# Optimization experiments

Hardware: AMD Instinct MI355X
Metric: run time of the kernel (lower is better)

The kernel has to match this reference:

```python
import jax, jax.numpy as jnp
import numpy as np

NUM_HEADS = 12


def setup_inputs() -> dict:
    key = jax.random.key(0)
    k0, k1, k2 = jax.random.split(key, 3)
    B, S, D = 2, 2048, 1536
    scale = 1.0 / np.sqrt(D)
    return {
        "hidden_states": jax.random.normal(k0, (B, S, D), dtype=jnp.float32),
        "W_fc": jax.random.normal(k1, (D, D), dtype=jnp.float32) * scale,
        "b_fc": jnp.zeros((D,), dtype=jnp.float32),
        "W_proj": jax.random.normal(k2, (D, D), dtype=jnp.float32) * scale,
        "b_proj": jnp.zeros((D,), dtype=jnp.float32),
    }


def reference(hidden_states, W_fc, b_fc, W_proj, b_proj):
    B, S, D = hidden_states.shape
    H = NUM_HEADS
    hd = D // H
    # value_states: [B, H, S, hd] (key_states == value_states in the original)
    v = (hidden_states @ W_fc.T + b_fc).reshape(B, S, H, hd).transpose(0, 2, 1, 3)
    # Uniform-weight causal sliding-window attention, window_h = 2^(h+1)-1.
    i = jnp.arange(S)[:, None]          # query pos
    j = jnp.arange(S)[None, :]          # key pos
    w = (2 ** jnp.arange(1, H + 1, dtype=jnp.int32) - 1)[:, None, None]  # [H,1,1]
    mask = (j <= i) & (j >= i - w + 1)                                    # [H,S,S]
    valid_len = jnp.minimum(i + 1, w).astype(v.dtype)                     # [H,S,1]
    attn = jnp.where(mask, 1.0 / valid_len, 0.0)                          # [H,S,S]
    # [H,S,S] x [B,H,S,hd] -> [B,S,H,hd] -> [B,S,D]
    out = jnp.einsum("hqk,bhkd->bqhd", attn, v).reshape(B, S, D)
    attn_weights = jnp.broadcast_to(attn[None], (B, H, S, S))
    return out @ W_proj.T + b_proj, attn_weights
```

## Files before the change

kernel.cpp:

```cpp
#include <hip/hip_runtime.h>
#include <hip/hip_bf16.h>

#define S_LEN   2048
#define DMODEL  1536
#define NBATCH  2
#define NHEADS  12
#define MROWS   (NBATCH * S_LEN)
#define NCHUNK  64
#define CHUNK   32

#define NGEMM_BLK  384
#define AW_BLK     3072
#define AW_TOTAL4  25165824u

#define AW_G1   10223616u
#define AW_PF    1572864u
#define AW_WA    3932160u
#define AW_G2    9437184u

#define PF_BLK   768
#define PF_AWBLK 1536
#define WA_BLK   3072
#define WA_AWBLK 1536

typedef unsigned short u16;
typedef __attribute__((ext_vector_type(8))) short bf16x8;
typedef __attribute__((ext_vector_type(4))) float f32x4;

__device__ __forceinline__ u16 f2bf(float x) {
  unsigned u = __float_as_uint(x);
  u += 0x7fffu + ((u >> 16) & 1u);
  return (u16)(u >> 16);
}
__device__ __forceinline__ float bf2f(u16 x) {
  return __uint_as_float(((unsigned)x) << 16);
}

__device__ __forceinline__ void aw_stream(f32x4* __restrict__ aw, unsigned aw0,
                                          unsigned awcnt, unsigned blk, unsigned nblk) {
  const unsigned stride = nblk * 256u;
  const unsigned end = aw0 + awcnt;
  unsigned t = aw0 + blk * 256u + threadIdx.x;
  for (; t < end; t += stride) {
    int j0 = (int)(t & 511u) << 2;
    int i  = (int)(t >> 9) & (S_LEN - 1);
    int bh = (int)(t >> 20);
    int h  = bh >= NHEADS ? bh - NHEADS : bh;
    int w  = (2 << h) - 1;
    int len = min(i + 1, w);
    float inv = 1.0f / (float)len;
    int lo = i - w + 1;
    f32x4 r;
    r.x = (j0     <= i && j0     >= lo) ? inv : 0.f;
    r.y = (j0 + 1 <= i && j0 + 1 >= lo) ? inv : 0.f;
    r.z = (j0 + 2 <= i && j0 + 2 >= lo) ? inv : 0.f;
    r.w = (j0 + 3 <= i && j0 + 3 >= lo) ? inv : 0.f;
    __builtin_nontemporal_store(r, &aw[t]);
  }
}

#define N4_HID  1572864
#define N4_W    589824
__global__ void cvt_all(const float4* __restrict__ h, const float4* __restrict__ wf,
                        const float4* __restrict__ wp, ushort4* __restrict__ ho,
                        ushort4* __restrict__ wfo, ushort4* __restrict__ wpo) {
  int t = blockIdx.x * blockDim.x + threadIdx.x;
  const float4* src;
  ushort4* dst;
  int idx;
  if (t < N4_HID)            { src = h;  dst = ho;  idx = t; }
  else if (t < N4_HID + N4_W){ src = wf; dst = wfo; idx = t - N4_HID; }
  else                       { src = wp; dst = wpo; idx = t - N4_HID - N4_W; }
  float4 f = src[idx];
  ushort4 o;
  o.x = f2bf(f.x); o.y = f2bf(f.y); o.z = f2bf(f.z); o.w = f2bf(f.w);
  dst[idx] = o;
}

__device__ __forceinline__ void gld_lds16(u16* lds, const u16* g) {
  __builtin_amdgcn_global_load_lds(
      (const __attribute__((address_space(1))) unsigned int*)g,
      (__attribute__((address_space(3))) unsigned int*)lds, 16, 0, 0);
}

template <bool WITH_CSUM, typename CT>
__global__ __launch_bounds__(256)
void gemm_aw(const u16* __restrict__ A, const u16* __restrict__ B,
             const float* __restrict__ bias, CT* __restrict__ C,
             float* __restrict__ cs, f32x4* __restrict__ aw,
             unsigned aw0, unsigned awcnt, int Ndim, int Kdim) {
  if ((int)blockIdx.x >= NGEMM_BLK) {
    aw_stream(aw, aw0, awcnt, blockIdx.x - NGEMM_BLK, gridDim.x - NGEMM_BLK);
    return;
  }

  __shared__ __align__(16) u16 As[2][128 * 32];
  __shared__ __align__(16) u16 Bs[2][128 * 32];
  __shared__ float colpart[4][128];

  const int tid  = threadIdx.x;
  const int wave = tid >> 6;
  const int lane = tid & 63;
  const int l15  = lane & 15;
  const int quad = lane >> 4;
  const int bm = (blockIdx.x / (DMODEL / 128)) * 128;
  const int bn = (blockIdx.x % (DMODEL / 128)) * 128;
  const int wm = (wave >> 1) * 64;
  const int wn = (wave & 1) * 64;

  f32x4 acc[4][4] = {};

  const int srow = wave * 32 + (lane >> 2);
  const int skk  = (lane & 3) * 8;
  const u16* gA = A + (size_t)(bm + srow) * Kdim + skk;
  const u16* gB = B + (size_t)(bn + srow) * Kdim + skk;
  const int lofs = (wave * 32) * 32;
  const size_t rstep16 = (size_t)16 * Kdim;

  gld_lds16(&As[0][lofs],           gA);
  gld_lds16(&As[0][lofs + 16 * 32], gA + rstep16);
  gld_lds16(&Bs[0][lofs],           gB);
  gld_lds16(&Bs[0][lofs + 16 * 32], gB + rstep16);

  int cur = 0;
  for (int k0 = 0; k0 < Kdim; k0 += 32) {
    __syncthreads();
    if (k0 + 32 < Kdim) {
      const int nxt = cur ^ 1;
      gld_lds16(&As[nxt][lofs],           gA + k0 + 32);
      gld_lds16(&As[nxt][lofs + 16 * 32], gA + k0 + 32 + rstep16);
      gld_lds16(&Bs[nxt][lofs],           gB + k0 + 32);
      gld_lds16(&Bs[nxt][lofs + 16 * 32], gB + k0 + 32 + rstep16);
    }

    bf16x8 af[4], bfr[4];
#pragma unroll
    for (int i = 0; i < 4; ++i)
      af[i] = *(const bf16x8*)&As[cur][(wm + i * 16 + l15) * 32 + quad * 8];
#pragma unroll
    for (int j = 0; j < 4; ++j)
      bfr[j] = *(const bf16x8*)&Bs[cur][(wn + j * 16 + l15) * 32 + quad * 8];
#pragma unroll
    for (int i = 0; i < 4; ++i)
#pragma unroll
      for (int j = 0; j < 4; ++j)
        acc[i][j] = __builtin_amdgcn_mfma_f32_16x16x32_bf16(af[i], bfr[j], acc[i][j], 0, 0, 0);
    cur ^= 1;
  }

  const int r0 = quad * 4;
#pragma unroll
  for (int j = 0; j < 4; ++j) {
    const int col = bn + wn + j * 16 + l15;
    const float bj = bias[col];
    float sA = 0.f, sB = 0.f;
#pragma unroll
    for (int i = 0; i < 4; ++i) {
      const int row = bm + wm + i * 16 + r0;
#pragma unroll
      for (int r = 0; r < 4; ++r) {
        float cv = acc[i][j][r] + bj;
        if constexpr (sizeof(CT) == 2) {
          C[(size_t)(row + r) * Ndim + col] = (CT)f2bf(cv);
        } else {
          __builtin_nontemporal_store((CT)cv, &C[(size_t)(row + r) * Ndim + col]);
        }
        if (WITH_CSUM) { if (i < 2) sA += cv; else sB += cv; }
      }
    }
    if (WITH_CSUM) {
      sA += __shfl_xor(sA, 16); sA += __shfl_xor(sA, 32);
      sB += __shfl_xor(sB, 16); sB += __shfl_xor(sB, 32);
      if (quad == 0) {
        colpart[(wm >> 5) | 0][wn + j * 16 + l15] = sA;
        colpart[(wm >> 5) | 1][wn + j * 16 + l15] = sB;
      }
    }
  }
  if (WITH_CSUM) {
    __syncthreads();
    if (tid < 128) {
      const int b  = bm >> 11;
      const int c0 = (bm & 2047) >> 5;
#pragma unroll
      for (int g = 0; g < 4; ++g)
        cs[((size_t)b * NCHUNK + c0 + g) * DMODEL + bn + tid] = colpart[g][tid];
    }
  }
}

__global__ void chunk_prefix_aw(const float* __restrict__ cs, float* __restrict__ E,
                                f32x4* __restrict__ aw, unsigned aw0, unsigned awcnt) {
  if ((int)blockIdx.x >= PF_BLK) {
    aw_stream(aw, aw0, awcnt, blockIdx.x - PF_BLK, PF_AWBLK);
    return;
  }
  int t = blockIdx.x * blockDim.x + threadIdx.x;
  int d = t % DMODEL;
  int c = (t / DMODEL) % NCHUNK;
  int b = t / (DMODEL * NCHUNK);
  const float* p = cs + (size_t)b * NCHUNK * DMODEL + d;
  float s = 0.f;
  for (int cc = 0; cc < c; ++cc) s += p[(size_t)cc * DMODEL];
  E[t] = s;
}

__global__ void winavg_aw(const u16* __restrict__ v, const float* __restrict__ E,
                          u16* __restrict__ A2,
                          f32x4* __restrict__ aw, unsigned aw0, unsigned awcnt) {
  if ((int)blockIdx.x >= WA_BLK) {
    aw_stream(aw, aw0, awcnt, blockIdx.x - WA_BLK, WA_AWBLK);
    return;
  }
  int t = blockIdx.x * blockDim.x + threadIdx.x;
  int d = t % DMODEL;
  int s = (t / DMODEL) & 255;
  int b = t / (DMODEL * 256);
  const int h = d >> 7;
  const int w = (2 << h) - 1;
  const u16* vb  = v + (size_t)b * S_LEN * DMODEL + d;
  const float* Eb = E + (size_t)b * NCHUNK * DMODEL + d;

  const int i0 = s * 8;
  float lead = Eb[(size_t)(i0 >> 5) * DMODEL];
  for (int r = i0 & ~31; r < i0; ++r)
    lead += bf2f(vb[(size_t)r * DMODEL]);

  float trail = 0.f;
  if (i0 + 7 >= w) {
    const int jf = max(i0, w) - w;
    if (jf > 0) {
      const int ct = (jf - 1) >> 5;
      trail = Eb[(size_t)ct * DMODEL];
      for (int r = ct * 32; r < jf; ++r)
        trail += bf2f(vb[(size_t)r * DMODEL]);
    }
  }

  u16* out = A2 + ((size_t)(b * S_LEN + i0)) * DMODEL + d;
#pragma unroll
  for (int rr = 0; rr < 8; ++rr) {
    const int i = i0 + rr;
    lead += bf2f(vb[(size_t)i * DMODEL]);
    float o;
    if (i < w) {
      o = lead / (float)(i + 1);
    } else {
      trail += bf2f(vb[(size_t)(i - w) * DMODEL]);
      o = (lead - trail) / (float)w;
    }
    out[(size_t)rr * DMODEL] = f2bf(o);
  }
}

extern "C" void kernel_launch(void* const* d_in, const int* in_sizes, int n_in,
                              void* d_out, int out_size, void* d_ws, size_t ws_size,
                              hipStream_t stream) {
  const float* hidden = (const float*)d_in[0];
  const float* W_fc   = (const float*)d_in[1];
  const float* b_fc   = (const float*)d_in[2];
  const float* W_proj = (const float*)d_in[3];
  const float* b_proj = (const float*)d_in[4];
  float* outp = (float*)d_out;
  f32x4* aw = (f32x4*)(outp + (size_t)MROWS * DMODEL);

  char* ws = (char*)d_ws;
  u16*   A16   = (u16*)(ws);
  u16*   Wfc16 = (u16*)(ws + 12582912);
  u16*   Wpj16 = (u16*)(ws + 17301504);
  u16*   v16   = (u16*)(ws + 22020096);
  float* csums = (float*)(ws + 34603008);
  float* Epre  = (float*)(ws + 35389440);

  cvt_all<<<10752, 256, 0, stream>>>((const float4*)hidden, (const float4*)W_fc,
                                     (const float4*)W_proj, (ushort4*)A16,
                                     (ushort4*)Wfc16, (ushort4*)Wpj16);

  gemm_aw<true, u16><<<NGEMM_BLK + AW_BLK, 256, 0, stream>>>(
      A16, Wfc16, b_fc, v16, csums, aw, 0u, AW_G1, DMODEL, DMODEL);

  chunk_prefix_aw<<<PF_BLK + PF_AWBLK, 256, 0, stream>>>(
      csums, Epre, aw, AW_G1, AW_PF);

  winavg_aw<<<WA_BLK + WA_AWBLK, 256, 0, stream>>>(
      v16, Epre, A16, aw, AW_G1 + AW_PF, AW_WA);

  gemm_aw<false, float><<<NGEMM_BLK + AW_BLK, 256, 0, stream>>>(
      A16, Wpj16, b_proj, outp, nullptr, aw, AW_G1 + AW_PF + AW_WA, AW_G2, DMODEL, DMODEL);
}
```

Baseline: 532.8 us.

## Drop chunk-prefix kernel, fold prefix sums into winavg, rebalance attn-weight streaming

Removes the separate chunk_prefix kernel: winavg now sums the per-chunk column sums directly, computing both the lead and trail prefixes in one pass. Attention-weight writing is widened to 8 floats per thread, and part of it moves into the conversion kernel, with the split across the four remaining launches re-tuned. This saves one launch and the round trip through the E buffer, and spreads the large output write over more of the timeline. In exchange each winavg thread makes up to 64 strided column-sum reads instead of one, which is redundant work.

```diff
diff --git a/kernel.cpp b/kernel.cpp
--- a/kernel.cpp
+++ b/kernel.cpp
@@ -7,21 +7,20 @@
 #define NHEADS  12
 #define MROWS   (NBATCH * S_LEN)
 #define NCHUNK  64
-#define CHUNK   32
 
 #define NGEMM_BLK  384
+
+#define AW_TOT8   12582912u
+#define AW_CVT8    1048576u
+#define AW_G1_8    4718592u
+#define AW_WA8     2359296u
+#define AW_G2_8    4456448u
+
+#define CVT_BLK    10752
+#define CVT_AWBLK  1024
 #define AW_BLK     3072
-#define AW_TOTAL4  25165824u
-
-#define AW_G1   10223616u
-#define AW_PF    1572864u
-#define AW_WA    3932160u
-#define AW_G2    9437184u
-
-#define PF_BLK   768
-#define PF_AWBLK 1536
-#define WA_BLK   3072
-#define WA_AWBLK 1536
+#define WA_BLK     3072
+#define WA_AWBLK   2048
 
 typedef unsigned short u16;
 typedef __attribute__((ext_vector_type(8))) short bf16x8;
@@ -36,26 +35,29 @@
   return __uint_as_float(((unsigned)x) << 16);
 }
 
-__device__ __forceinline__ void aw_stream(f32x4* __restrict__ aw, unsigned aw0,
-                                          unsigned awcnt, unsigned blk, unsigned nblk) {
+__device__ __forceinline__ void aw_stream8(f32x4* __restrict__ aw, unsigned aw0,
+                                           unsigned awcnt, unsigned blk, unsigned nblk) {
   const unsigned stride = nblk * 256u;
   const unsigned end = aw0 + awcnt;
-  unsigned t = aw0 + blk * 256u + threadIdx.x;
-  for (; t < end; t += stride) {
-    int j0 = (int)(t & 511u) << 2;
-    int i  = (int)(t >> 9) & (S_LEN - 1);
-    int bh = (int)(t >> 20);
+  for (unsigned t = aw0 + blk * 256u + threadIdx.x; t < end; t += stride) {
+    int j0 = (int)(t & 255u) << 3;
+    int i  = (int)(t >> 8) & (S_LEN - 1);
+    int bh = (int)(t >> 19);
     int h  = bh >= NHEADS ? bh - NHEADS : bh;
     int w  = (2 << h) - 1;
-    int len = min(i + 1, w);
-    float inv = 1.0f / (float)len;
+    float inv = 1.0f / (float)min(i + 1, w);
     int lo = i - w + 1;
-    f32x4 r;
-    r.x = (j0     <= i && j0     >= lo) ? inv : 0.f;
-    r.y = (j0 + 1 <= i && j0 + 1 >= lo) ? inv : 0.f;
-    r.z = (j0 + 2 <= i && j0 + 2 >= lo) ? inv : 0.f;
-    r.w = (j0 + 3 <= i && j0 + 3 >= lo) ? inv : 0.f;
-    __builtin_nontemporal_store(r, &aw[t]);
+    f32x4 r0, r1;
+    r0.x = (j0     <= i && j0     >= lo) ? inv : 0.f;
+    r0.y = (j0 + 1 <= i && j0 + 1 >= lo) ? inv : 0.f;
+    r0.z = (j0 + 2 <= i && j0 + 2 >= lo) ? inv : 0.f;
+    r0.w = (j0 + 3 <= i && j0 + 3 >= lo) ? inv : 0.f;
+    r1.x = (j0 + 4 <= i && j0 + 4 >= lo) ? inv : 0.f;
+    r1.y = (j0 + 5 <= i && j0 + 5 >= lo) ? inv : 0.f;
+    r1.z = (j0 + 6 <= i && j0 + 6 >= lo) ? inv : 0.f;
+    r1.w = (j0 + 7 <= i && j0 + 7 >= lo) ? inv : 0.f;
+    __builtin_nontemporal_store(r0, &aw[2u * t]);
+    __builtin_nontemporal_store(r1, &aw[2u * t + 1u]);
   }
 }
 
@@ -63,7 +65,12 @@
 #define N4_W    589824
 __global__ void cvt_all(const float4* __restrict__ h, const float4* __restrict__ wf,
                         const float4* __restrict__ wp, ushort4* __restrict__ ho,
-                        ushort4* __restrict__ wfo, ushort4* __restrict__ wpo) {
+                        ushort4* __restrict__ wfo, ushort4* __restrict__ wpo,
+                        f32x4* __restrict__ aw, unsigned aw0, unsigned awcnt) {
+  if ((int)blockIdx.x >= CVT_BLK) {
+    aw_stream8(aw, aw0, awcnt, blockIdx.x - CVT_BLK, CVT_AWBLK);
+    return;
+  }
   int t = blockIdx.x * blockDim.x + threadIdx.x;
   const float4* src;
   ushort4* dst;
@@ -90,7 +97,7 @@
              float* __restrict__ cs, f32x4* __restrict__ aw,
              unsigned aw0, unsigned awcnt, int Ndim, int Kdim) {
   if ((int)blockIdx.x >= NGEMM_BLK) {
-    aw_stream(aw, aw0, awcnt, blockIdx.x - NGEMM_BLK, gridDim.x - NGEMM_BLK);
+    aw_stream8(aw, aw0, awcnt, blockIdx.x - NGEMM_BLK, gridDim.x - NGEMM_BLK);
     return;
   }
 
@@ -189,27 +196,11 @@
   }
 }
 
-__global__ void chunk_prefix_aw(const float* __restrict__ cs, float* __restrict__ E,
-                                f32x4* __restrict__ aw, unsigned aw0, unsigned awcnt) {
-  if ((int)blockIdx.x >= PF_BLK) {
-    aw_stream(aw, aw0, awcnt, blockIdx.x - PF_BLK, PF_AWBLK);
-    return;
-  }
-  int t = blockIdx.x * blockDim.x + threadIdx.x;
-  int d = t % DMODEL;
-  int c = (t / DMODEL) % NCHUNK;
-  int b = t / (DMODEL * NCHUNK);
-  const float* p = cs + (size_t)b * NCHUNK * DMODEL + d;
-  float s = 0.f;
-  for (int cc = 0; cc < c; ++cc) s += p[(size_t)cc * DMODEL];
-  E[t] = s;
-}
-
-__global__ void winavg_aw(const u16* __restrict__ v, const float* __restrict__ E,
+__global__ void winavg_aw(const u16* __restrict__ v, const float* __restrict__ cs,
                           u16* __restrict__ A2,
                           f32x4* __restrict__ aw, unsigned aw0, unsigned awcnt) {
   if ((int)blockIdx.x >= WA_BLK) {
-    aw_stream(aw, aw0, awcnt, blockIdx.x - WA_BLK, WA_AWBLK);
+    aw_stream8(aw, aw0, awcnt, blockIdx.x - WA_BLK, WA_AWBLK);
     return;
   }
   int t = blockIdx.x * blockDim.x + threadIdx.x;
@@ -219,22 +210,29 @@
   const int h = d >> 7;
   const int w = (2 << h) - 1;
   const u16* vb  = v + (size_t)b * S_LEN * DMODEL + d;
-  const float* Eb = E + (size_t)b * NCHUNK * DMODEL + d;
+  const float* cb = cs + (size_t)b * NCHUNK * DMODEL + d;
 
   const int i0 = s * 8;
-  float lead = Eb[(size_t)(i0 >> 5) * DMODEL];
-  for (int r = i0 & ~31; r < i0; ++r)
+  const int clead = i0 >> 5;
+
+  int jf = 0, ct = 0;
+  const bool ht = (i0 + 7 >= w);
+  if (ht) { jf = max(i0, w) - w; ct = jf > 0 ? (jf - 1) >> 5 : 0; }
+
+  float lead = 0.f, tb = 0.f;
+  for (int cc = 0; cc < clead; ++cc) {
+    float x = cb[(size_t)cc * DMODEL];
+    lead += x;
+    if (cc < ct) tb += x;
+  }
+  for (int r = clead * 32; r < i0; ++r)
     lead += bf2f(vb[(size_t)r * DMODEL]);
 
   float trail = 0.f;
-  if (i0 + 7 >= w) {
-    const int jf = max(i0, w) - w;
-    if (jf > 0) {
-      const int ct = (jf - 1) >> 5;
-      trail = Eb[(size_t)ct * DMODEL];
-      for (int r = ct * 32; r < jf; ++r)
-        trail += bf2f(vb[(size_t)r * DMODEL]);
-    }
+  if (ht && jf > 0) {
+    trail = tb;
+    for (int r = ct * 32; r < jf; ++r)
+      trail += bf2f(vb[(size_t)r * DMODEL]);
   }
 
   u16* out = A2 + ((size_t)(b * S_LEN + i0)) * DMODEL + d;
@@ -270,21 +268,19 @@
   u16*   Wpj16 = (u16*)(ws + 17301504);
   u16*   v16   = (u16*)(ws + 22020096);
   float* csums = (float*)(ws + 34603008);
-  float* Epre  = (float*)(ws + 35389440);
-
-  cvt_all<<<10752, 256, 0, stream>>>((const float4*)hidden, (const float4*)W_fc,
-                                     (const float4*)W_proj, (ushort4*)A16,
-                                     (ushort4*)Wfc16, (ushort4*)Wpj16);
+
+  cvt_all<<<CVT_BLK + CVT_AWBLK, 256, 0, stream>>>(
+      (const float4*)hidden, (const float4*)W_fc, (const float4*)W_proj,
+      (ushort4*)A16, (ushort4*)Wfc16, (ushort4*)Wpj16,
+      aw, 0u, AW_CVT8);
 
   gemm_aw<true, u16><<<NGEMM_BLK + AW_BLK, 256, 0, stream>>>(
-      A16, Wfc16, b_fc, v16, csums, aw, 0u, AW_G1, DMODEL, DMODEL);
-
-  chunk_prefix_aw<<<PF_BLK + PF_AWBLK, 256, 0, stream>>>(
-      csums, Epre, aw, AW_G1, AW_PF);
+      A16, Wfc16, b_fc, v16, csums, aw, AW_CVT8, AW_G1_8, DMODEL, DMODEL);
 
   winavg_aw<<<WA_BLK + WA_AWBLK, 256, 0, stream>>>(
-      v16, Epre, A16, aw, AW_G1 + AW_PF, AW_WA);
+      v16, csums, A16, aw, AW_CVT8 + AW_G1_8, AW_WA8);
 
   gemm_aw<false, float><<<NGEMM_BLK + AW_BLK, 256, 0, stream>>>(
-      A16, Wpj16, b_proj, outp, nullptr, aw, AW_G1 + AW_PF + AW_WA, AW_G2, DMODEL, DMODEL);
-}
+      A16, Wpj16, b_proj, outp, nullptr, aw,
+      AW_CVT8 + AW_G1_8 + AW_WA8, AW_G2_8, DMODEL, DMODEL);
+}
```

New measurement: 566.5 us. +6.3%, slower.
